# Kernel optimization log

Measured on AMD Instinct MI355X. Metric: run time of the kernel, lower is better.

## Reference

```python
import jax, jax.numpy as jnp
import numpy as np

B, S, D, H = 8, 2048, 1024, 4
HD = D // H


def _layernorm(x, w, b, eps=1e-5):
    mu = jnp.mean(x, axis=-1, keepdims=True)
    var = jnp.mean((x - mu) ** 2, axis=-1, keepdims=True)
    return (x - mu) * jax.lax.rsqrt(var + eps) * w + b


def setup_inputs() -> dict:
    key = jax.random.key(0)
    ks = jax.random.split(key, 10)
    s = 1.0 / np.sqrt(D)
    return {
        "text_representation": jax.random.normal(ks[0], (B, S, D), jnp.float32),
        "image_representation": jax.random.normal(ks[1], (B, S, D), jnp.float32),
        "ln_t_w": jnp.ones((D,), jnp.float32),
        "ln_t_b": jnp.zeros((D,), jnp.float32),
        "ln_i_w": jnp.ones((D,), jnp.float32),
        "ln_i_b": jnp.zeros((D,), jnp.float32),
        "Wa": jax.random.uniform(ks[2], (H, HD, D), jnp.float32, -s, s),
        "Wa_b": jax.random.uniform(ks[3], (H, HD), jnp.float32, -s, s),
        "Wq": jax.random.uniform(ks[4], (H, HD, D), jnp.float32, -s, s),
        "Wq_b": jax.random.uniform(ks[5], (H, HD), jnp.float32, -s, s),
        "sim_w": jax.random.uniform(ks[6], (HD, 1), jnp.float32, -1.0, 1.0),
        "sim_b": jax.random.uniform(ks[7], (HD,), jnp.float32, -1.0, 1.0),
        "fc_w": jax.random.uniform(ks[8], (1, H * HD), jnp.float32, -s, s),
        "fc_b": jax.random.uniform(ks[9], (1,), jnp.float32, -s, s),
    }


def reference(text_representation, image_representation, ln_t_w, ln_t_b,
              ln_i_w, ln_i_b, Wa, Wa_b, Wq, Wq_b, sim_w, sim_b, fc_w, fc_b):
    eps_cos = 1e-6
    text_rep = _layernorm(text_representation, ln_t_w, ln_t_b)   # [B,S,D]
    image_rep = _layernorm(image_representation, ln_i_w, ln_i_b)  # [B,S,D]
    # cosine similarity along last dim (torch-style norm clamping)
    tn = jnp.maximum(jnp.linalg.norm(text_rep, axis=-1), eps_cos)
    im = jnp.maximum(jnp.linalg.norm(image_rep, axis=-1), eps_cos)
    per_pos_sim = jnp.sum(text_rep * image_rep, axis=-1) / (tn * im)  # [B,S]
    global_sim = jnp.mean(per_pos_sim, axis=1, keepdims=True)          # [B,1]
    text_global = jnp.mean(text_rep, axis=1)    # [B,D]
    image_global = jnp.mean(image_rep, axis=1)  # [B,D]
    gate_a = jnp.einsum('bd,hkd->bhk', text_global, Wa) + Wa_b    # [B,H,HD]
    gate_q = jnp.einsum('bd,hkd->bhk', image_global, Wq) + Wq_b   # [B,H,HD]
    sim_feat = global_sim * sim_w[:, 0] + sim_b                   # [B,HD]
    gates = jax.nn.relu(gate_a + gate_q + sim_feat[:, None, :])   # [B,H,HD]
    combined = gates.reshape(gates.shape[0], H * HD)              # [B,H*HD]
    final_gate = jax.nn.sigmoid(combined @ fc_w.T + fc_b)         # [B,1]
    g = final_gate[:, :, None]                                    # [B,1,1]
    return g * text_rep + (1.0 - g) * image_rep
```

## Files before the change

### kernel.cpp

```cpp
#include <hip/hip_runtime.h>
#include <math.h>

#define BB 8
#define SS 2048
#define DD 1024
#define HH 4
#define HDD 256
#define NROW (BB*SS)
#define G 8
#define NSLICE (NROW/G)

#define OFF_MU_T 0
#define OFF_RS_T NROW
#define OFF_MU_I (2*NROW)
#define OFF_RS_I (3*NROW)
#define OFF_PT   (4*NROW)
#define OFF_PI   (OFF_PT + NSLICE*DD)
#define OFF_PS   (OFF_PI + NSLICE*DD)
#define OFF_TG   (OFF_PS + NSLICE)
#define OFF_IG   (OFF_TG + BB*DD)
#define OFF_SIM  (OFF_IG + BB*DD)
#define OFF_LOGIT (OFF_SIM + BB)

__device__ __forceinline__ float wred(float v) {
#pragma unroll
  for (int m = 32; m > 0; m >>= 1) v += __shfl_xor(v, m, 64);
  return v;
}

__global__ __launch_bounds__(256) void k1_stats(
    const float* __restrict__ text, const float* __restrict__ image,
    const float* __restrict__ wt, const float* __restrict__ bt,
    const float* __restrict__ wi, const float* __restrict__ bi,
    float* __restrict__ ws)
{
  const int g    = blockIdx.x;
  const int tid  = threadIdx.x;
  const int lane = tid & 63;
  const int wv   = tid >> 6;
  const int d0   = tid << 2;
  const int row0 = g * G;

  __shared__ float red1[4][4];
  __shared__ float red2[4][4];

  const float4 wt4 = *(const float4*)(wt + d0);
  const float4 bt4 = *(const float4*)(bt + d0);
  const float4 wi4 = *(const float4*)(wi + d0);
  const float4 bi4 = *(const float4*)(bi + d0);

  float4 tga = make_float4(0.f,0.f,0.f,0.f);
  float4 iga = make_float4(0.f,0.f,0.f,0.f);
  float sim_loc = 0.f;

  float4 ct = *(const float4*)(text  + (size_t)row0*DD + d0);
  float4 ci = *(const float4*)(image + (size_t)row0*DD + d0);

  for (int r = 0; r < G; ++r) {
    float4 nt_ = ct, ni_ = ci;
    if (r + 1 < G) {
      nt_ = *(const float4*)(text  + (size_t)(row0+r+1)*DD + d0);
      ni_ = *(const float4*)(image + (size_t)(row0+r+1)*DD + d0);
    }
    float s1 = ct.x + ct.y + ct.z + ct.w;
    float s2 = ct.x*ct.x + ct.y*ct.y + ct.z*ct.z + ct.w*ct.w;
    float s3 = ci.x + ci.y + ci.z + ci.w;
    float s4 = ci.x*ci.x + ci.y*ci.y + ci.z*ci.z + ci.w*ci.w;
    s1 = wred(s1); s2 = wred(s2); s3 = wred(s3); s4 = wred(s4);
    if (lane == 0) { red1[wv][0]=s1; red1[wv][1]=s2; red1[wv][2]=s3; red1[wv][3]=s4; }
    __syncthreads();
    const float st  = red1[0][0]+red1[1][0]+red1[2][0]+red1[3][0];
    const float sst = red1[0][1]+red1[1][1]+red1[2][1]+red1[3][1];
    const float si  = red1[0][2]+red1[1][2]+red1[2][2]+red1[3][2];
    const float ssi = red1[0][3]+red1[1][3]+red1[2][3]+red1[3][3];
    const float invD = 1.f/DD;
    const float mt = st*invD,  vt = sst*invD - mt*mt;
    const float mi = si*invD,  vi = ssi*invD - mi*mi;
    const float rt = rsqrtf(vt + 1e-5f);
    const float ri = rsqrtf(vi + 1e-5f);
    if (tid == 0) {
      const int row = row0 + r;
      ws[OFF_MU_T+row]=mt; ws[OFF_RS_T+row]=rt;
      ws[OFF_MU_I+row]=mi; ws[OFF_RS_I+row]=ri;
    }
    float4 tn, in_;
    tn.x  = (ct.x-mt)*rt*wt4.x + bt4.x;  tn.y  = (ct.y-mt)*rt*wt4.y + bt4.y;
    tn.z  = (ct.z-mt)*rt*wt4.z + bt4.z;  tn.w  = (ct.w-mt)*rt*wt4.w + bt4.w;
    in_.x = (ci.x-mi)*ri*wi4.x + bi4.x;  in_.y = (ci.y-mi)*ri*wi4.y + bi4.y;
    in_.z = (ci.z-mi)*ri*wi4.z + bi4.z;  in_.w = (ci.w-mi)*ri*wi4.w + bi4.w;
    tga.x += tn.x; tga.y += tn.y; tga.z += tn.z; tga.w += tn.w;
    iga.x += in_.x; iga.y += in_.y; iga.z += in_.z; iga.w += in_.w;
    float dv  = tn.x*in_.x + tn.y*in_.y + tn.z*in_.z + tn.w*in_.w;
    float nt2 = tn.x*tn.x + tn.y*tn.y + tn.z*tn.z + tn.w*tn.w;
    float ni2 = in_.x*in_.x + in_.y*in_.y + in_.z*in_.z + in_.w*in_.w;
    dv = wred(dv); nt2 = wred(nt2); ni2 = wred(ni2);
    if (lane == 0) { red2[wv][0]=dv; red2[wv][1]=nt2; red2[wv][2]=ni2; }
    __syncthreads();
    if (tid == 0) {
      const float d_all = red2[0][0]+red2[1][0]+red2[2][0]+red2[3][0];
      const float nt = fmaxf(sqrtf(red2[0][1]+red2[1][1]+red2[2][1]+red2[3][1]), 1e-6f);
      const float ni = fmaxf(sqrtf(red2[0][2]+red2[1][2]+red2[2][2]+red2[3][2]), 1e-6f);
      sim_loc += d_all / (nt*ni);
    }
    ct = nt_; ci = ni_;
  }
  *(float4*)(ws + OFF_PT + (size_t)g*DD + d0) = tga;
  *(float4*)(ws + OFF_PI + (size_t)g*DD + d0) = iga;
  if (tid == 0) ws[OFF_PS + g] = sim_loc;
}

__global__ __launch_bounds__(256) void kR_reduce(float* __restrict__ ws)
{
  const int tid = threadIdx.x;
  if (blockIdx.x < 32) {
    const int b  = blockIdx.x >> 2;
    const int ch = blockIdx.x & 3;
    const int d  = ch*256 + tid;
    const float* pt = ws + OFF_PT + (size_t)(b*256)*DD + d;
    const float* pi = ws + OFF_PI + (size_t)(b*256)*DD + d;
    float at = 0.f, ai = 0.f;
#pragma unroll 4
    for (int s = 0; s < 256; ++s) {
      at += pt[(size_t)s*DD];
      ai += pi[(size_t)s*DD];
    }
    ws[OFF_TG + b*DD + d] = at;
    ws[OFF_IG + b*DD + d] = ai;
  } else {
    __shared__ float sred[256];
    const int b = tid >> 5, j = tid & 31;
    float a = 0.f;
#pragma unroll
    for (int k = 0; k < 8; ++k) a += ws[OFF_PS + b*256 + j*8 + k];
    sred[tid] = a;
    __syncthreads();
    if (j == 0) {
      float s = 0.f;
#pragma unroll
      for (int m = 0; m < 32; ++m) s += sred[b*32 + m];
      ws[OFF_SIM + b] = s;
    }
    if (tid < BB) ws[OFF_LOGIT + tid] = 0.f;
  }
}

__global__ __launch_bounds__(256) void k2_gates(
    const float* __restrict__ Wa, const float* __restrict__ Wab,
    const float* __restrict__ Wq, const float* __restrict__ Wqb,
    const float* __restrict__ simw, const float* __restrict__ simb,
    const float* __restrict__ fcw, float* __restrict__ ws)
{
  const int tid  = threadIdx.x;
  const int lane = tid & 63;
  const int wv   = tid >> 6;
  const int r0   = blockIdx.x * 4;
  const int d0   = tid << 2;

  __shared__ float red[4][4][BB];

  for (int rr = 0; rr < 4; ++rr) {
    const int r = r0 + rr;
    const float4 a4 = *(const float4*)(Wa + (size_t)r*DD + d0);
    const float4 q4 = *(const float4*)(Wq + (size_t)r*DD + d0);
    float acc[BB];
#pragma unroll
    for (int b = 0; b < BB; ++b) {
      const float4 t = *(const float4*)(ws + OFF_TG + b*DD + d0);
      const float4 i = *(const float4*)(ws + OFF_IG + b*DD + d0);
      acc[b] = a4.x*t.x + a4.y*t.y + a4.z*t.z + a4.w*t.w
             + q4.x*i.x + q4.y*i.y + q4.z*i.z + q4.w*i.w;
    }
#pragma unroll
    for (int b = 0; b < BB; ++b) {
      acc[b] = wred(acc[b]);
      if (lane == 0) red[rr][wv][b] = acc[b];
    }
  }
  __syncthreads();
  if (tid < BB) {
    const int b = tid;
    const float inv = 1.f/SS;
    const float gs = ws[OFF_SIM + b] * inv;
    float part = 0.f;
#pragma unroll
    for (int rr = 0; rr < 4; ++rr) {
      const int r = r0 + rr;
      const int k = r & 255;
      const float v = (red[rr][0][b] + red[rr][1][b] + red[rr][2][b] + red[rr][3][b]) * inv;
      float gate = v + Wab[r] + Wqb[r] + gs*simw[k] + simb[k];
      gate = fmaxf(gate, 0.f);
      part += gate * fcw[r];
    }
    atomicAdd(&ws[OFF_LOGIT + b], part);
  }
}

__global__ __launch_bounds__(256) void k3_blend(
    const float* __restrict__ text, const float* __restrict__ image,
    const float* __restrict__ wt, const float* __restrict__ bt,
    const float* __restrict__ wi, const float* __restrict__ bi,
    const float* __restrict__ fcb,
    const float* __restrict__ ws, float* __restrict__ out)
{
  const int r0 = blockIdx.x * 2;
  const int b  = r0 >> 11;
  const int d0 = threadIdx.x << 2;

  const float4 ta = *(const float4*)(text  + (size_t)r0*DD + d0);
  const float4 ia = *(const float4*)(image + (size_t)r0*DD + d0);
  const float4 tb = *(const float4*)(text  + (size_t)(r0+1)*DD + d0);
  const float4 ib = *(const float4*)(image + (size_t)(r0+1)*DD + d0);
  const float4 wt4 = *(const float4*)(wt + d0);
  const float4 bt4 = *(const float4*)(bt + d0);
  const float4 wi4 = *(const float4*)(wi + d0);
  const float4 bi4 = *(const float4*)(bi + d0);

  const float g  = 1.f / (1.f + expf(-(ws[OFF_LOGIT+b] + fcb[0])));
  const float gi = 1.f - g;

  const float mta = ws[OFF_MU_T+r0],   rta = ws[OFF_RS_T+r0];
  const float mia = ws[OFF_MU_I+r0],   ria = ws[OFF_RS_I+r0];
  const float mtb = ws[OFF_MU_T+r0+1], rtb = ws[OFF_RS_T+r0+1];
  const float mib = ws[OFF_MU_I+r0+1], rib = ws[OFF_RS_I+r0+1];

  const float gta = g*rta, gia = gi*ria;
  const float gtb = g*rtb, gib = gi*rib;

  float4 oa, ob;
  oa.x = gta*(ta.x-mta)*wt4.x + g*bt4.x + gia*(ia.x-mia)*wi4.x + gi*bi4.x;
  oa.y = gta*(ta.y-mta)*wt4.y + g*bt4.y + gia*(ia.y-mia)*wi4.y + gi*bi4.y;
  oa.z = gta*(ta.z-mta)*wt4.z + g*bt4.z + gia*(ia.z-mia)*wi4.z + gi*bi4.z;
  oa.w = gta*(ta.w-mta)*wt4.w + g*bt4.w + gia*(ia.w-mia)*wi4.w + gi*bi4.w;
  ob.x = gtb*(tb.x-mtb)*wt4.x + g*bt4.x + gib*(ib.x-mib)*wi4.x + gi*bi4.x;
  ob.y = gtb*(tb.y-mtb)*wt4.y + g*bt4.y + gib*(ib.y-mib)*wi4.y + gi*bi4.y;
  ob.z = gtb*(tb.z-mtb)*wt4.z + g*bt4.z + gib*(ib.z-mib)*wi4.z + gi*bi4.z;
  ob.w = gtb*(tb.w-mtb)*wt4.w + g*bt4.w + gib*(ib.w-mib)*wi4.w + gi*bi4.w;

  *(float4*)(out + (size_t)r0*DD + d0)     = oa;
  *(float4*)(out + (size_t)(r0+1)*DD + d0) = ob;
}

extern "C" void kernel_launch(void* const* d_in, const int* in_sizes, int n_in,
                              void* d_out, int out_size, void* d_ws, size_t ws_size,
                              hipStream_t stream)
{
  const float* text   = (const float*)d_in[0];
  const float* image  = (const float*)d_in[1];
  const float* ln_t_w = (const float*)d_in[2];
  const float* ln_t_b = (const float*)d_in[3];
  const float* ln_i_w = (const float*)d_in[4];
  const float* ln_i_b = (const float*)d_in[5];
  const float* Wa     = (const float*)d_in[6];
  const float* Wab    = (const float*)d_in[7];
  const float* Wq     = (const float*)d_in[8];
  const float* Wqb    = (const float*)d_in[9];
  const float* simw   = (const float*)d_in[10];
  const float* simb   = (const float*)d_in[11];
  const float* fcw    = (const float*)d_in[12];
  const float* fcb    = (const float*)d_in[13];
  float* ws  = (float*)d_ws;
  float* out = (float*)d_out;

  k1_stats<<<NSLICE, 256, 0, stream>>>(text, image, ln_t_w, ln_t_b, ln_i_w, ln_i_b, ws);
  kR_reduce<<<33, 256, 0, stream>>>(ws);
  k2_gates<<<HH*HDD/4, 256, 0, stream>>>(Wa, Wab, Wq, Wqb, simw, simb, fcw, ws);
  k3_blend<<<NROW/2, 256, 0, stream>>>(text, image, ln_t_w, ln_t_b, ln_i_w, ln_i_b, fcb, ws, out);
}
```

Before: 272.2 us.

## Process row pairs in stats kernel, widen reduce grid, blend four rows per block

Result: faster. 245.1 us (-10.0%).

```diff
diff --git a/kernel.cpp b/kernel.cpp
--- a/kernel.cpp
+++ b/kernel.cpp
@@ -28,6 +28,12 @@
   return v;
 }
 
+__device__ __forceinline__ float hsum(const float4 v) { return v.x+v.y+v.z+v.w; }
+__device__ __forceinline__ float hsq(const float4 v)  { return v.x*v.x+v.y*v.y+v.z*v.z+v.w*v.w; }
+__device__ __forceinline__ float hdot(const float4 a, const float4 b) {
+  return a.x*b.x + a.y*b.y + a.z*b.z + a.w*b.w;
+}
+
 __global__ __launch_bounds__(256) void k1_stats(
     const float* __restrict__ text, const float* __restrict__ image,
     const float* __restrict__ wt, const float* __restrict__ bt,
@@ -41,8 +47,8 @@
   const int d0   = tid << 2;
   const int row0 = g * G;
 
-  __shared__ float red1[4][4];
-  __shared__ float red2[4][4];
+  __shared__ float red1[4][8];
+  __shared__ float red2[4][6];
 
   const float4 wt4 = *(const float4*)(wt + d0);
   const float4 bt4 = *(const float4*)(bt + d0);
@@ -53,56 +59,69 @@
   float4 iga = make_float4(0.f,0.f,0.f,0.f);
   float sim_loc = 0.f;
 
-  float4 ct = *(const float4*)(text  + (size_t)row0*DD + d0);
-  float4 ci = *(const float4*)(image + (size_t)row0*DD + d0);
-
-  for (int r = 0; r < G; ++r) {
-    float4 nt_ = ct, ni_ = ci;
-    if (r + 1 < G) {
-      nt_ = *(const float4*)(text  + (size_t)(row0+r+1)*DD + d0);
-      ni_ = *(const float4*)(image + (size_t)(row0+r+1)*DD + d0);
-    }
-    float s1 = ct.x + ct.y + ct.z + ct.w;
-    float s2 = ct.x*ct.x + ct.y*ct.y + ct.z*ct.z + ct.w*ct.w;
-    float s3 = ci.x + ci.y + ci.z + ci.w;
-    float s4 = ci.x*ci.x + ci.y*ci.y + ci.z*ci.z + ci.w*ci.w;
-    s1 = wred(s1); s2 = wred(s2); s3 = wred(s3); s4 = wred(s4);
-    if (lane == 0) { red1[wv][0]=s1; red1[wv][1]=s2; red1[wv][2]=s3; red1[wv][3]=s4; }
-    __syncthreads();
-    const float st  = red1[0][0]+red1[1][0]+red1[2][0]+red1[3][0];
-    const float sst = red1[0][1]+red1[1][1]+red1[2][1]+red1[3][1];
-    const float si  = red1[0][2]+red1[1][2]+red1[2][2]+red1[3][2];
-    const float ssi = red1[0][3]+red1[1][3]+red1[2][3]+red1[3][3];
+  for (int r = 0; r < G; r += 2) {
+    const size_t base0 = (size_t)(row0 + r) * DD + d0;
+    const size_t base1 = base0 + DD;
+    const float4 t0 = *(const float4*)(text  + base0);
+    const float4 i0 = *(const float4*)(image + base0);
+    const float4 t1 = *(const float4*)(text  + base1);
+    const float4 i1 = *(const float4*)(image + base1);
+
+    float a0 = hsum(t0), a1 = hsq(t0), a2 = hsum(i0), a3 = hsq(i0);
+    float a4 = hsum(t1), a5 = hsq(t1), a6 = hsum(i1), a7 = hsq(i1);
+    a0 = wred(a0); a1 = wred(a1); a2 = wred(a2); a3 = wred(a3);
+    a4 = wred(a4); a5 = wred(a5); a6 = wred(a6); a7 = wred(a7);
+    if (lane == 0) {
+      red1[wv][0]=a0; red1[wv][1]=a1; red1[wv][2]=a2; red1[wv][3]=a3;
+      red1[wv][4]=a4; red1[wv][5]=a5; red1[wv][6]=a6; red1[wv][7]=a7;
+    }
+    __syncthreads();
+    float s[8];
+#pragma unroll
+    for (int q = 0; q < 8; ++q) s[q] = red1[0][q]+red1[1][q]+red1[2][q]+red1[3][q];
     const float invD = 1.f/DD;
-    const float mt = st*invD,  vt = sst*invD - mt*mt;
-    const float mi = si*invD,  vi = ssi*invD - mi*mi;
-    const float rt = rsqrtf(vt + 1e-5f);
-    const float ri = rsqrtf(vi + 1e-5f);
+    const float mt0 = s[0]*invD, rt0 = rsqrtf(s[1]*invD - mt0*mt0 + 1e-5f);
+    const float mi0 = s[2]*invD, ri0 = rsqrtf(s[3]*invD - mi0*mi0 + 1e-5f);
+    const float mt1 = s[4]*invD, rt1 = rsqrtf(s[5]*invD - mt1*mt1 + 1e-5f);
+    const float mi1 = s[6]*invD, ri1 = rsqrtf(s[7]*invD - mi1*mi1 + 1e-5f);
     if (tid == 0) {
       const int row = row0 + r;
-      ws[OFF_MU_T+row]=mt; ws[OFF_RS_T+row]=rt;
-      ws[OFF_MU_I+row]=mi; ws[OFF_RS_I+row]=ri;
-    }
-    float4 tn, in_;
-    tn.x  = (ct.x-mt)*rt*wt4.x + bt4.x;  tn.y  = (ct.y-mt)*rt*wt4.y + bt4.y;
-    tn.z  = (ct.z-mt)*rt*wt4.z + bt4.z;  tn.w  = (ct.w-mt)*rt*wt4.w + bt4.w;
-    in_.x = (ci.x-mi)*ri*wi4.x + bi4.x;  in_.y = (ci.y-mi)*ri*wi4.y + bi4.y;
-    in_.z = (ci.z-mi)*ri*wi4.z + bi4.z;  in_.w = (ci.w-mi)*ri*wi4.w + bi4.w;
-    tga.x += tn.x; tga.y += tn.y; tga.z += tn.z; tga.w += tn.w;
-    iga.x += in_.x; iga.y += in_.y; iga.z += in_.z; iga.w += in_.w;
-    float dv  = tn.x*in_.x + tn.y*in_.y + tn.z*in_.z + tn.w*in_.w;
-    float nt2 = tn.x*tn.x + tn.y*tn.y + tn.z*tn.z + tn.w*tn.w;
-    float ni2 = in_.x*in_.x + in_.y*in_.y + in_.z*in_.z + in_.w*in_.w;
-    dv = wred(dv); nt2 = wred(nt2); ni2 = wred(ni2);
-    if (lane == 0) { red2[wv][0]=dv; red2[wv][1]=nt2; red2[wv][2]=ni2; }
+      ws[OFF_MU_T+row]=mt0;   ws[OFF_RS_T+row]=rt0;
+      ws[OFF_MU_I+row]=mi0;   ws[OFF_RS_I+row]=ri0;
+      ws[OFF_MU_T+row+1]=mt1; ws[OFF_RS_T+row+1]=rt1;
+      ws[OFF_MU_I+row+1]=mi1; ws[OFF_RS_I+row+1]=ri1;
+    }
+    float4 tn0, in0, tn1, in1;
+    tn0.x = (t0.x-mt0)*rt0*wt4.x + bt4.x;  tn0.y = (t0.y-mt0)*rt0*wt4.y + bt4.y;
+    tn0.z = (t0.z-mt0)*rt0*wt4.z + bt4.z;  tn0.w = (t0.w-mt0)*rt0*wt4.w + bt4.w;
+    in0.x = (i0.x-mi0)*ri0*wi4.x + bi4.x;  in0.y = (i0.y-mi0)*ri0*wi4.y + bi4.y;
+    in0.z = (i0.z-mi0)*ri0*wi4.z + bi4.z;  in0.w = (i0.w-mi0)*ri0*wi4.w + bi4.w;
+    tn1.x = (t1.x-mt1)*rt1*wt4.x + bt4.x;  tn1.y = (t1.y-mt1)*rt1*wt4.y + bt4.y;
+    tn1.z = (t1.z-mt1)*rt1*wt4.z + bt4.z;  tn1.w = (t1.w-mt1)*rt1*wt4.w + bt4.w;
+    in1.x = (i1.x-mi1)*ri1*wi4.x + bi4.x;  in1.y = (i1.y-mi1)*ri1*wi4.y + bi4.y;
+    in1.z = (i1.z-mi1)*ri1*wi4.z + bi4.z;  in1.w = (i1.w-mi1)*ri1*wi4.w + bi4.w;
+
+    tga.x += tn0.x + tn1.x; tga.y += tn0.y + tn1.y;
+    tga.z += tn0.z + tn1.z; tga.w += tn0.w + tn1.w;
+    iga.x += in0.x + in1.x; iga.y += in0.y + in1.y;
+    iga.z += in0.z + in1.z; iga.w += in0.w + in1.w;
+
+    float b0 = hdot(tn0,in0), b1 = hsq(tn0), b2 = hsq(in0);
+    float b3 = hdot(tn1,in1), b4 = hsq(tn1), b5 = hsq(in1);
+    b0 = wred(b0); b1 = wred(b1); b2 = wred(b2);
+    b3 = wred(b3); b4 = wred(b4); b5 = wred(b5);
+    if (lane == 0) {
+      red2[wv][0]=b0; red2[wv][1]=b1; red2[wv][2]=b2;
+      red2[wv][3]=b3; red2[wv][4]=b4; red2[wv][5]=b5;
+    }
     __syncthreads();
     if (tid == 0) {
-      const float d_all = red2[0][0]+red2[1][0]+red2[2][0]+red2[3][0];
-      const float nt = fmaxf(sqrtf(red2[0][1]+red2[1][1]+red2[2][1]+red2[3][1]), 1e-6f);
-      const float ni = fmaxf(sqrtf(red2[0][2]+red2[1][2]+red2[2][2]+red2[3][2]), 1e-6f);
-      sim_loc += d_all / (nt*ni);
-    }
-    ct = nt_; ci = ni_;
+      float u[6];
+#pragma unroll
+      for (int q = 0; q < 6; ++q) u[q] = red2[0][q]+red2[1][q]+red2[2][q]+red2[3][q];
+      sim_loc += u[0] / (fmaxf(sqrtf(u[1]),1e-6f) * fmaxf(sqrtf(u[2]),1e-6f));
+      sim_loc += u[3] / (fmaxf(sqrtf(u[4]),1e-6f) * fmaxf(sqrtf(u[5]),1e-6f));
+    }
   }
   *(float4*)(ws + OFF_PT + (size_t)g*DD + d0) = tga;
   *(float4*)(ws + OFF_PI + (size_t)g*DD + d0) = iga;
@@ -112,20 +131,36 @@
 __global__ __launch_bounds__(256) void kR_reduce(float* __restrict__ ws)
 {
   const int tid = threadIdx.x;
-  if (blockIdx.x < 32) {
-    const int b  = blockIdx.x >> 2;
-    const int ch = blockIdx.x & 3;
-    const int d  = ch*256 + tid;
-    const float* pt = ws + OFF_PT + (size_t)(b*256)*DD + d;
-    const float* pi = ws + OFF_PI + (size_t)(b*256)*DD + d;
+  if (blockIdx.x < 256) {
+    const int b   = blockIdx.x >> 5;
+    const int ch  = blockIdx.x & 31;
+    const int cl  = tid & 31;
+    const int sg  = tid >> 5;
+    const int col = ch*32 + cl;
+    const float* pt = ws + OFF_PT + (size_t)(b*256 + sg*32)*DD + col;
+    const float* pi = ws + OFF_PI + (size_t)(b*256 + sg*32)*DD + col;
     float at = 0.f, ai = 0.f;
 #pragma unroll 4
-    for (int s = 0; s < 256; ++s) {
-      at += pt[(size_t)s*DD];
-      ai += pi[(size_t)s*DD];
-    }
-    ws[OFF_TG + b*DD + d] = at;
-    ws[OFF_IG + b*DD + d] = ai;
+    for (int k = 0; k < 32; ++k) {
+      at += pt[(size_t)k*DD];
+      ai += pi[(size_t)k*DD];
+    }
+    __shared__ float sred[2][8][32];
+    sred[0][sg][cl] = at;
+    sred[1][sg][cl] = ai;
+    __syncthreads();
+    if (tid < 32) {
+      float v = 0.f;
+#pragma unroll
+      for (int q = 0; q < 8; ++q) v += sred[0][q][tid];
+      ws[OFF_TG + b*DD + ch*32 + tid] = v;
+    } else if (tid < 64) {
+      const int c = tid - 32;
+      float v = 0.f;
+#pragma unroll
+      for (int q = 0; q < 8; ++q) v += sred[1][q][c];
+      ws[OFF_IG + b*DD + ch*32 + c] = v;
+    }
   } else {
     __shared__ float sred[256];
     const int b = tid >> 5, j = tid & 31;
@@ -167,8 +202,7 @@
     for (int b = 0; b < BB; ++b) {
       const float4 t = *(const float4*)(ws + OFF_TG + b*DD + d0);
       const float4 i = *(const float4*)(ws + OFF_IG + b*DD + d0);
-      acc[b] = a4.x*t.x + a4.y*t.y + a4.z*t.z + a4.w*t.w
-             + q4.x*i.x + q4.y*i.y + q4.z*i.z + q4.w*i.w;
+      acc[b] = hdot(a4, t) + hdot(q4, i);
     }
 #pragma unroll
     for (int b = 0; b < BB; ++b) {
@@ -202,14 +236,16 @@
     const float* __restrict__ fcb,
     const float* __restrict__ ws, float* __restrict__ out)
 {
-  const int r0 = blockIdx.x * 2;
+  const int r0 = blockIdx.x * 4;
   const int b  = r0 >> 11;
   const int d0 = threadIdx.x << 2;
 
-  const float4 ta = *(const float4*)(text  + (size_t)r0*DD + d0);
-  const float4 ia = *(const float4*)(image + (size_t)r0*DD + d0);
-  const float4 tb = *(const float4*)(text  + (size_t)(r0+1)*DD + d0);
-  const float4 ib = *(const float4*)(image + (size_t)(r0+1)*DD + d0);
+  float4 t[4], im[4];
+#pragma unroll
+  for (int r = 0; r < 4; ++r) {
+    t[r]  = *(const float4*)(text  + (size_t)(r0+r)*DD + d0);
+    im[r] = *(const float4*)(image + (size_t)(r0+r)*DD + d0);
+  }
   const float4 wt4 = *(const float4*)(wt + d0);
   const float4 bt4 = *(const float4*)(bt + d0);
   const float4 wi4 = *(const float4*)(wi + d0);
@@ -218,26 +254,18 @@
   const float g  = 1.f / (1.f + expf(-(ws[OFF_LOGIT+b] + fcb[0])));
   const float gi = 1.f - g;
 
-  const float mta = ws[OFF_MU_T+r0],   rta = ws[OFF_RS_T+r0];
-  const float mia = ws[OFF_MU_I+r0],   ria = ws[OFF_RS_I+r0];
-  const float mtb = ws[OFF_MU_T+r0+1], rtb = ws[OFF_RS_T+r0+1];
-  const float mib = ws[OFF_MU_I+r0+1], rib = ws[OFF_RS_I+r0+1];
-
-  const float gta = g*rta, gia = gi*ria;
-  const float gtb = g*rtb, gib = gi*rib;
-
-  float4 oa, ob;
-  oa.x = gta*(ta.x-mta)*wt4.x + g*bt4.x + gia*(ia.x-mia)*wi4.x + gi*bi4.x;
-  oa.y = gta*(ta.y-mta)*wt4.y + g*bt4.y + gia*(ia.y-mia)*wi4.y + gi*bi4.y;
-  oa.z = gta*(ta.z-mta)*wt4.z + g*bt4.z + gia*(ia.z-mia)*wi4.z + gi*bi4.z;
-  oa.w = gta*(ta.w-mta)*wt4.w + g*bt4.w + gia*(ia.w-mia)*wi4.w + gi*bi4.w;
-  ob.x = gtb*(tb.x-mtb)*wt4.x + g*bt4.x + gib*(ib.x-mib)*wi4.x + gi*bi4.x;
-  ob.y = gtb*(tb.y-mtb)*wt4.y + g*bt4.y + gib*(ib.y-mib)*wi4.y + gi*bi4.y;
-  ob.z = gtb*(tb.z-mtb)*wt4.z + g*bt4.z + gib*(ib.z-mib)*wi4.z + gi*bi4.z;
-  ob.w = gtb*(tb.w-mtb)*wt4.w + g*bt4.w + gib*(ib.w-mib)*wi4.w + gi*bi4.w;
-
-  *(float4*)(out + (size_t)r0*DD + d0)     = oa;
-  *(float4*)(out + (size_t)(r0+1)*DD + d0) = ob;
+#pragma unroll
+  for (int r = 0; r < 4; ++r) {
+    const float mt = ws[OFF_MU_T+r0+r], rt = ws[OFF_RS_T+r0+r];
+    const float mi = ws[OFF_MU_I+r0+r], ri = ws[OFF_RS_I+r0+r];
+    const float gt = g*rt, gii = gi*ri;
+    float4 o;
+    o.x = gt*(t[r].x-mt)*wt4.x + g*bt4.x + gii*(im[r].x-mi)*wi4.x + gi*bi4.x;
+    o.y = gt*(t[r].y-mt)*wt4.y + g*bt4.y + gii*(im[r].y-mi)*wi4.y + gi*bi4.y;
+    o.z = gt*(t[r].z-mt)*wt4.z + g*bt4.z + gii*(im[r].z-mi)*wi4.z + gi*bi4.z;
+    o.w = gt*(t[r].w-mt)*wt4.w + g*bt4.w + gii*(im[r].w-mi)*wi4.w + gi*bi4.w;
+    *(float4*)(out + (size_t)(r0+r)*DD + d0) = o;
+  }
 }
 
 extern "C" void kernel_launch(void* const* d_in, const int* in_sizes, int n_in,
@@ -262,7 +290,7 @@
   float* out = (float*)d_out;
 
   k1_stats<<<NSLICE, 256, 0, stream>>>(text, image, ln_t_w, ln_t_b, ln_i_w, ln_i_b, ws);
-  kR_reduce<<<33, 256, 0, stream>>>(ws);
+  kR_reduce<<<257, 256, 0, stream>>>(ws);
   k2_gates<<<HH*HDD/4, 256, 0, stream>>>(Wa, Wab, Wq, Wqb, simw, simb, fcw, ws);
-  k3_blend<<<NROW/2, 256, 0, stream>>>(text, image, ln_t_w, ln_t_b, ln_i_w, ln_i_b, fcb, ws, out);
-}
+  k3_blend<<<NROW/4, 256, 0, stream>>>(text, image, ln_t_w, ln_t_b, ln_i_w, ln_i_b, fcb, ws, out);
+}
```
